# Kernel tuning notes

Measured on AMD Instinct MI355X. Metric: run time of the kernel, lower is better.

The kernel has to match this reference:

```python
import jax, jax.numpy as jnp
import numpy as np

N_NODES = 100000
N_EDGES = 50000
NNZ = 1600000
C_IN = 128
C_OUT = 128
BN_EPS = 1e-5


def setup_inputs() -> dict:
    key = jax.random.key(0)
    k_x, k_ni, k_ei, k_w, k_W, k_b = jax.random.split(key, 6)
    x = jax.random.normal(k_x, (N_NODES, C_IN), dtype=jnp.float32)
    node_idx = jax.random.randint(k_ni, (NNZ,), 0, N_NODES, dtype=jnp.int64)
    edge_idx = jax.random.randint(k_ei, (NNZ,), 0, N_EDGES, dtype=jnp.int64)
    hyperedge_index = jnp.stack([node_idx, edge_idx], axis=0)  # [2, nnz]
    hyperedge_weight = jax.random.uniform(k_w, (N_EDGES,), dtype=jnp.float32)
    W = jax.random.normal(k_W, (C_IN, C_OUT), dtype=jnp.float32) * (1.0 / np.sqrt(C_IN))
    b = jax.random.normal(k_b, (C_OUT,), dtype=jnp.float32) * 0.02
    gamma = jnp.ones((C_OUT,), dtype=jnp.float32)
    beta = jnp.zeros((C_OUT,), dtype=jnp.float32)
    return {"x": x, "hyperedge_index": hyperedge_index,
            "hyperedge_weight": hyperedge_weight, "W": W, "b": b,
            "gamma": gamma, "beta": beta}


def reference(x, hyperedge_index, hyperedge_weight, W, b, gamma, beta):
    # HypergraphConv (PyG semantics): out = D^{-1} H B^{-1} H^T (X W) + b
    # D_v = sum_{e: v in e} w_e  (hyperedge weights enter via node degree),
    # B_e = |e| (number of incident nodes).
    N = x.shape[0]
    E = hyperedge_weight.shape[0]
    node_idx = hyperedge_index[0]
    edge_idx = hyperedge_index[1]

    xt = x @ W  # [N, C_out]

    # Node degree D (weighted) and hyperedge degree B.
    D = jax.ops.segment_sum(hyperedge_weight[edge_idx], node_idx, num_segments=N)
    D_inv = jnp.where(D > 0, 1.0 / D, 0.0)  # inf -> 0
    Bdeg = jax.ops.segment_sum(jnp.ones(edge_idx.shape, dtype=xt.dtype),
                               edge_idx, num_segments=E)
    B_inv = jnp.where(Bdeg > 0, 1.0 / Bdeg, 0.0)

    # node -> hyperedge aggregation: e = B^{-1} sum_{v in e} xt_v
    e_feat = jax.ops.segment_sum(xt[node_idx], edge_idx, num_segments=E)
    e_feat = e_feat * B_inv[:, None]  # [E, C_out]

    # hyperedge -> node aggregation: out_v = D^{-1} sum_{e ni v} e_feat_e
    out = jax.ops.segment_sum(e_feat[edge_idx], node_idx, num_segments=N)
    out = out * D_inv[:, None] + b  # [N, C_out]

    # BatchNorm (training-mode batch statistics over nodes)
    mean = jnp.mean(out, axis=0)
    var = jnp.mean(jnp.square(out - mean), axis=0)  # biased, as BatchNorm1d
    out = (out - mean) * jax.lax.rsqrt(var + BN_EPS) * gamma + beta

    # SiLU activation
    out = out * jax.nn.sigmoid(out)
    # NOTE: original code computes `x = out + x` for the skip but returns `out`,
    # so the skip is a no-op; we faithfully return `out` (use_skip=False here).
    return out
```

## Files before the change

### kernel.cpp

```cpp
#include <hip/hip_runtime.h>
#include <cstdint>
#include <cstddef>

#define CC 128
#define LOG_FINE 7
#define FINE 128
#define CAPE 6144
#define CAPV 3072
#define BIN_TILE 8192

typedef __attribute__((ext_vector_type(8))) short bf16x8;
typedef __attribute__((ext_vector_type(4))) float f32x4;

__device__ __forceinline__ unsigned f2b(float f) {
    const unsigned u = __float_as_uint(f);
    return (u + 0x7fffu + ((u >> 16) & 1u)) >> 16;
}
__device__ __forceinline__ float b2f_lo(unsigned u) { return __uint_as_float(u << 16); }
__device__ __forceinline__ float b2f_hi(unsigned u) { return __uint_as_float(u & 0xffff0000u); }

__global__ __launch_bounds__(512) void prep(const int* __restrict__ nidx,
                                            const int* __restrict__ eidx,
                                            int* __restrict__ curE,
                                            int* __restrict__ curV,
                                            unsigned* __restrict__ binnedE,
                                            unsigned* __restrict__ binnedV,
                                            int nnz, int nbE, int nbV, int nbin,
                                            const float4* __restrict__ xin,
                                            uint2* __restrict__ xh, int n4) {
    __shared__ int cntE[512], gposE[512];
    __shared__ int cntV[1024], gposV[1024];
    const int tid = threadIdx.x;
    if (blockIdx.x >= (unsigned)nbin) {
        const int bid = blockIdx.x - nbin;
        const int nblk = gridDim.x - nbin;
        for (int i = bid * 512 + tid; i < n4; i += nblk * 512) {
            const float4 v = xin[i];
            xh[i] = make_uint2(f2b(v.x) | (f2b(v.y) << 16), f2b(v.z) | (f2b(v.w) << 16));
        }
        return;
    }
    for (int i = tid; i < nbE; i += 512) cntE[i] = 0;
    for (int i = tid; i < nbV; i += 512) cntV[i] = 0;
    __syncthreads();
    const int base = blockIdx.x * BIN_TILE;
    int pE[16], rE[16], pV[16], rV[16];
#pragma unroll
    for (int j = 0; j < 16; ++j) {
        const int i = base + tid + j * 512;
        if (i < nnz) {
            const int e = eidx[i], v = nidx[i];
            const int bE = e >> LOG_FINE, bV = v >> LOG_FINE;
            rE[j] = (bE << 16) | atomicAdd(&cntE[bE], 1);
            pE[j] = (v << LOG_FINE) | (e & (FINE - 1));
            rV[j] = (bV << 16) | atomicAdd(&cntV[bV], 1);
            pV[j] = (e << LOG_FINE) | (v & (FINE - 1));
        } else { rE[j] = -1; rV[j] = -1; }
    }
    __syncthreads();
    for (int i = tid; i < nbE; i += 512) {
        const int c = cntE[i];
        gposE[i] = (c > 0) ? atomicAdd(&curE[i], c) : 0;
    }
    for (int i = tid; i < nbV; i += 512) {
        const int c = cntV[i];
        gposV[i] = (c > 0) ? atomicAdd(&curV[i], c) : 0;
    }
    __syncthreads();
#pragma unroll
    for (int j = 0; j < 16; ++j) {
        if (rE[j] >= 0) {
            const int b = rE[j] >> 16;
            binnedE[(size_t)b * CAPE + gposE[b] + (rE[j] & 0xffff)] = (unsigned)pE[j];
        }
        if (rV[j] >= 0) {
            const int b = rV[j] >> 16;
            binnedV[(size_t)b * CAPV + gposV[b] + (rV[j] & 0xffff)] = (unsigned)pV[j];
        }
    }
}

__global__ __launch_bounds__(256) void bfrag_prep(const float* __restrict__ W,
                                                  uint4* __restrict__ Bfrag) {
    const int idx = blockIdx.x * 256 + threadIdx.x;
    if (idx >= 2048) return;
    const int lane = idx & 63, t = idx >> 6;
    const int kk = t >> 3, nt = t & 7;
    const int k0 = kk * 32 + (lane >> 4) * 8;
    const int n = nt * 16 + (lane & 15);
    unsigned r[4];
#pragma unroll
    for (int p = 0; p < 4; ++p) {
        const float w0 = W[(size_t)(k0 + 2 * p) * CC + n];
        const float w1 = W[(size_t)(k0 + 2 * p + 1) * CC + n];
        r[p] = f2b(w0) | (f2b(w1) << 16);
    }
    Bfrag[idx] = make_uint4(r[0], r[1], r[2], r[3]);
}

__global__ __launch_bounds__(512) void fill_fineE(const int* __restrict__ cur,
                                                  unsigned* __restrict__ binned,
                                                  int2* __restrict__ rows, int nrows) {
    __shared__ unsigned vals[CAPE];
    __shared__ int scnt[FINE], soff[FINE], sscan[FINE];
    const int tid = threadIdx.x;
    const int b = blockIdx.x;
    const int base = b * CAPE;
    const int cnt = cur[b];
    for (int i = tid; i < cnt; i += 512) vals[i] = binned[base + i];
    if (tid < FINE) scnt[tid] = 0;
    __syncthreads();
    for (int i = tid; i < cnt; i += 512) atomicAdd(&scnt[vals[i] & (FINE - 1)], 1);
    __syncthreads();
    if (tid < FINE) sscan[tid] = scnt[tid];
    __syncthreads();
#pragma unroll
    for (int d = 1; d < FINE; d <<= 1) {
        int t = 0;
        if (tid >= d && tid < FINE) t = sscan[tid - d];
        __syncthreads();
        if (tid < FINE) sscan[tid] += t;
        __syncthreads();
    }
    if (tid < FINE) {
        const int excl = sscan[tid] - scnt[tid];
        soff[tid] = excl;
        const int row = (b << LOG_FINE) + tid;
        if (row < nrows) rows[row] = make_int2(base + excl, base + excl + scnt[tid]);
    }
    __syncthreads();
    for (int i = tid; i < cnt; i += 512) {
        const unsigned p = vals[i];
        const int slot = (int)(p & (FINE - 1));
        const int pos = base + atomicAdd(&soff[slot], 1);
        binned[pos] = p >> LOG_FINE;
    }
}

__global__ __launch_bounds__(512) void fillV_gather(const int* __restrict__ curV,
                                                    unsigned* __restrict__ binnedV,
                                                    const float* __restrict__ hw,
                                                    int2* __restrict__ rowsV,
                                                    float* __restrict__ Dinv,
                                                    int N, int nbV,
                                                    const int2* __restrict__ rowsE,
                                                    const unsigned* __restrict__ binnedE,
                                                    const uint4* __restrict__ xh4,
                                                    uint4* __restrict__ eraw4, int E) {
    __shared__ unsigned vals[CAPV];
    __shared__ int scnt[FINE], soff[FINE], sscan[FINE];
    __shared__ float sd[FINE];
    const int tid = threadIdx.x;
    if (blockIdx.x < (unsigned)nbV) {
        const int b = blockIdx.x;
        const int base = b * CAPV;
        const int cnt = curV[b];
        for (int i = tid; i < cnt; i += 512) vals[i] = binnedV[base + i];
        if (tid < FINE) { scnt[tid] = 0; sd[tid] = 0.f; }
        __syncthreads();
        for (int i = tid; i < cnt; i += 512) atomicAdd(&scnt[vals[i] & (FINE - 1)], 1);
        __syncthreads();
        if (tid < FINE) sscan[tid] = scnt[tid];
        __syncthreads();
#pragma unroll
        for (int d = 1; d < FINE; d <<= 1) {
            int t = 0;
            if (tid >= d && tid < FINE) t = sscan[tid - d];
            __syncthreads();
            if (tid < FINE) sscan[tid] += t;
            __syncthreads();
        }
        if (tid < FINE) {
            const int excl = sscan[tid] - scnt[tid];
            soff[tid] = excl;
            const int row = (b << LOG_FINE) + tid;
            if (row < N) rowsV[row] = make_int2(base + excl, base + excl + scnt[tid]);
        }
        __syncthreads();
        for (int i = tid; i < cnt; i += 512) {
            const unsigned p = vals[i];
            const int slot = (int)(p & (FINE - 1));
            const int e = (int)(p >> LOG_FINE);
            const int pos = base + atomicAdd(&soff[slot], 1);
            binnedV[pos] = (unsigned)e;
            atomicAdd(&sd[slot], hw[e]);
        }
        __syncthreads();
        if (tid < FINE) {
            const int row = (b << LOG_FINE) + tid;
            if (row < N) {
                const float d = sd[tid];
                Dinv[row] = (d > 0.f) ? 1.f / d : 0.f;
            }
        }
        return;
    }
    const int sub = tid >> 5;
    const int half = (tid >> 4) & 1;
    const int q = tid & 15;
    const int e = (blockIdx.x - nbV) * 16 + sub;
    if (e >= E) return;
    const int2 st = rowsE[e];
    const int s = st.x, t = st.y;
    float a[8];
#pragma unroll
    for (int k = 0; k < 8; ++k) a[k] = 0.f;
    int j = s;
    for (; j + 7 < t; j += 8) {
        const int v0 = (int)binnedE[j + 0 + half];
        const int v1 = (int)binnedE[j + 2 + half];
        const int v2 = (int)binnedE[j + 4 + half];
        const int v3 = (int)binnedE[j + 6 + half];
        const uint4 u0 = xh4[(size_t)v0 * 16 + q];
        const uint4 u1 = xh4[(size_t)v1 * 16 + q];
        const uint4 u2 = xh4[(size_t)v2 * 16 + q];
        const uint4 u3 = xh4[(size_t)v3 * 16 + q];
        a[0] += b2f_lo(u0.x) + b2f_lo(u1.x) + b2f_lo(u2.x) + b2f_lo(u3.x);
        a[1] += b2f_hi(u0.x) + b2f_hi(u1.x) + b2f_hi(u2.x) + b2f_hi(u3.x);
        a[2] += b2f_lo(u0.y) + b2f_lo(u1.y) + b2f_lo(u2.y) + b2f_lo(u3.y);
        a[3] += b2f_hi(u0.y) + b2f_hi(u1.y) + b2f_hi(u2.y) + b2f_hi(u3.y);
        a[4] += b2f_lo(u0.z) + b2f_lo(u1.z) + b2f_lo(u2.z) + b2f_lo(u3.z);
        a[5] += b2f_hi(u0.z) + b2f_hi(u1.z) + b2f_hi(u2.z) + b2f_hi(u3.z);
        a[6] += b2f_lo(u0.w) + b2f_lo(u1.w) + b2f_lo(u2.w) + b2f_lo(u3.w);
        a[7] += b2f_hi(u0.w) + b2f_hi(u1.w) + b2f_hi(u2.w) + b2f_hi(u3.w);
    }
    for (; j + 1 < t; j += 2) {
        const int v0 = (int)binnedE[j + half];
        const uint4 u = xh4[(size_t)v0 * 16 + q];
        a[0] += b2f_lo(u.x); a[1] += b2f_hi(u.x);
        a[2] += b2f_lo(u.y); a[3] += b2f_hi(u.y);
        a[4] += b2f_lo(u.z); a[5] += b2f_hi(u.z);
        a[6] += b2f_lo(u.w); a[7] += b2f_hi(u.w);
    }
    if (j < t && half == 0) {
        const uint4 u = xh4[(size_t)binnedE[j] * 16 + q];
        a[0] += b2f_lo(u.x); a[1] += b2f_hi(u.x);
        a[2] += b2f_lo(u.y); a[3] += b2f_hi(u.y);
        a[4] += b2f_lo(u.z); a[5] += b2f_hi(u.z);
        a[6] += b2f_lo(u.w); a[7] += b2f_hi(u.w);
    }
#pragma unroll
    for (int k = 0; k < 8; ++k) a[k] += __shfl_xor(a[k], 16);
    if (half == 0) {
        const float binv = (t > s) ? 1.f / (float)(t - s) : 0.f;
#pragma unroll
        for (int k = 0; k < 8; ++k) a[k] *= binv;
        uint4 o;
        o.x = f2b(a[0]) | (f2b(a[1]) << 16);
        o.y = f2b(a[2]) | (f2b(a[3]) << 16);
        o.z = f2b(a[4]) | (f2b(a[5]) << 16);
        o.w = f2b(a[6]) | (f2b(a[7]) << 16);
        eraw4[(size_t)e * 16 + q] = o;
    }
}

__global__ __launch_bounds__(256) void mm_mfma(const uint4* __restrict__ A4,
                                               const uint4* __restrict__ Bfrag,
                                               unsigned short* __restrict__ Out, int M) {
    const int lane = threadIdx.x & 63;
    const int wave = threadIdx.x >> 6;
    const int row0 = blockIdx.x * 64 + wave * 16;
    const int g = lane >> 4;
    const int c = lane & 15;
    const int arow = row0 + c;
    uint4 a[4];
#pragma unroll
    for (int kk = 0; kk < 4; ++kk) {
        a[kk] = (arow < M) ? A4[(size_t)arow * 16 + kk * 4 + g]
                           : make_uint4(0u, 0u, 0u, 0u);
    }
    f32x4 acc[8];
#pragma unroll
    for (int nt = 0; nt < 8; ++nt) acc[nt] = (f32x4){0.f, 0.f, 0.f, 0.f};
#pragma unroll
    for (int nt = 0; nt < 8; ++nt) {
#pragma unroll
        for (int kk = 0; kk < 4; ++kk) {
            const uint4 bv = Bfrag[(kk * 8 + nt) * 64 + lane];
            acc[nt] = __builtin_amdgcn_mfma_f32_16x16x32_bf16(
                *(const bf16x8*)&a[kk], *(const bf16x8*)&bv, acc[nt], 0, 0, 0);
        }
    }
#pragma unroll
    for (int nt = 0; nt < 8; ++nt) {
#pragma unroll
        for (int r = 0; r < 4; ++r) {
            const int row = row0 + g * 4 + r;
            if (row < M) Out[(size_t)row * CC + nt * 16 + c] = (unsigned short)f2b(acc[nt][r]);
        }
    }
}

__global__ __launch_bounds__(256) void gather_e2n_bn(const int2* __restrict__ rows,
                                                     const unsigned* __restrict__ lst,
                                                     const uint4* __restrict__ ef4,
                                                     const float* __restrict__ Dinv,
                                                     const float* __restrict__ b,
                                                     uint4* __restrict__ oh,
                                                     float* __restrict__ copies, int N) {
    __shared__ float bl[8][256];
    const int tid = threadIdx.x;
    for (int i = tid; i < 2048; i += 256) ((float*)bl)[i] = 0.f;
    __syncthreads();
    const int sub = tid >> 5;
    const int half = (tid >> 4) & 1;
    const int q = tid & 15;
    const int v = blockIdx.x * 8 + sub;
    if (v < N) {
        const int2 st = rows[v];
        const int s = st.x, t = st.y;
        float a[8];
#pragma unroll
        for (int k = 0; k < 8; ++k) a[k] = 0.f;
        int j = s;
        for (; j + 7 < t; j += 8) {
            const int e0 = (int)lst[j + 0 + half];
            const int e1 = (int)lst[j + 2 + half];
            const int e2 = (int)lst[j + 4 + half];
            const int e3 = (int)lst[j + 6 + half];
            const uint4 u0 = ef4[(size_t)e0 * 16 + q];
            const uint4 u1 = ef4[(size_t)e1 * 16 + q];
            const uint4 u2 = ef4[(size_t)e2 * 16 + q];
            const uint4 u3 = ef4[(size_t)e3 * 16 + q];
            a[0] += b2f_lo(u0.x) + b2f_lo(u1.x) + b2f_lo(u2.x) + b2f_lo(u3.x);
            a[1] += b2f_hi(u0.x) + b2f_hi(u1.x) + b2f_hi(u2.x) + b2f_hi(u3.x);
            a[2] += b2f_lo(u0.y) + b2f_lo(u1.y) + b2f_lo(u2.y) + b2f_lo(u3.y);
            a[3] += b2f_hi(u0.y) + b2f_hi(u1.y) + b2f_hi(u2.y) + b2f_hi(u3.y);
            a[4] += b2f_lo(u0.z) + b2f_lo(u1.z) + b2f_lo(u2.z) + b2f_lo(u3.z);
            a[5] += b2f_hi(u0.z) + b2f_hi(u1.z) + b2f_hi(u2.z) + b2f_hi(u3.z);
            a[6] += b2f_lo(u0.w) + b2f_lo(u1.w) + b2f_lo(u2.w) + b2f_lo(u3.w);
            a[7] += b2f_hi(u0.w) + b2f_hi(u1.w) + b2f_hi(u2.w) + b2f_hi(u3.w);
        }
        for (; j + 1 < t; j += 2) {
            const int e0 = (int)lst[j + half];
            const uint4 u = ef4[(size_t)e0 * 16 + q];
            a[0] += b2f_lo(u.x); a[1] += b2f_hi(u.x);
            a[2] += b2f_lo(u.y); a[3] += b2f_hi(u.y);
            a[4] += b2f_lo(u.z); a[5] += b2f_hi(u.z);
            a[6] += b2f_lo(u.w); a[7] += b2f_hi(u.w);
        }
        if (j < t && half == 0) {
            const uint4 u = ef4[(size_t)lst[j] * 16 + q];
            a[0] += b2f_lo(u.x); a[1] += b2f_hi(u.x);
            a[2] += b2f_lo(u.y); a[3] += b2f_hi(u.y);
            a[4] += b2f_lo(u.z); a[5] += b2f_hi(u.z);
            a[6] += b2f_lo(u.w); a[7] += b2f_hi(u.w);
        }
#pragma unroll
        for (int k = 0; k < 8; ++k) a[k] += __shfl_xor(a[k], 16);
        if (half == 0) {
            const float dinv = Dinv[v];
            const float4 b0 = *(const float4*)&b[8 * q];
            const float4 b1 = *(const float4*)&b[8 * q + 4];
            float o[8];
            o[0] = a[0] * dinv + b0.x; o[1] = a[1] * dinv + b0.y;
            o[2] = a[2] * dinv + b0.z; o[3] = a[3] * dinv + b0.w;
            o[4] = a[4] * dinv + b1.x; o[5] = a[5] * dinv + b1.y;
            o[6] = a[6] * dinv + b1.z; o[7] = a[7] * dinv + b1.w;
            uint4 ov;
            ov.x = f2b(o[0]) | (f2b(o[1]) << 16);
            ov.y = f2b(o[2]) | (f2b(o[3]) << 16);
            ov.z = f2b(o[4]) | (f2b(o[5]) << 16);
            ov.w = f2b(o[6]) | (f2b(o[7]) << 16);
            oh[(size_t)v * 16 + q] = ov;
            *(float4*)&bl[sub][8 * q]       = make_float4(o[0], o[1], o[2], o[3]);
            *(float4*)&bl[sub][8 * q + 4]   = make_float4(o[4], o[5], o[6], o[7]);
            *(float4*)&bl[sub][128 + 8 * q] = make_float4(o[0] * o[0], o[1] * o[1],
                                                          o[2] * o[2], o[3] * o[3]);
            *(float4*)&bl[sub][132 + 8 * q] = make_float4(o[4] * o[4], o[5] * o[5],
                                                          o[6] * o[6], o[7] * o[7]);
        }
    }
    __syncthreads();
    float s = 0.f;
#pragma unroll
    for (int i = 0; i < 8; ++i) s += bl[i][tid];
    atomicAdd(&copies[(blockIdx.x & 63) * 256 + tid], s);
}

__global__ __launch_bounds__(256) void bn_silu(const uint2* __restrict__ oh2,
                                               const float* __restrict__ copies,
                                               const float* __restrict__ gamma,
                                               const float* __restrict__ beta,
                                               float* __restrict__ out, int N) {
    __shared__ float sl[256];
    const int tid = threadIdx.x;
    float s = 0.f;
#pragma unroll 8
    for (int i = 0; i < 64; ++i) s += copies[i * 256 + tid];
    sl[tid] = s;
    __syncthreads();
    const int sub = tid >> 5;
    const int lane = tid & 31;
    const int c4 = lane * 4;
    const float invN = 1.0f / (float)N;
    float g[4], bb[4];
#pragma unroll
    for (int k = 0; k < 4; ++k) {
        const float mean = sl[c4 + k] * invN;
        float var = sl[128 + c4 + k] * invN - mean * mean;
        var = fmaxf(var, 0.f);
        const float istd = rsqrtf(var + 1e-5f);
        g[k] = gamma[c4 + k] * istd;
        bb[k] = beta[c4 + k] - mean * g[k];
    }
    for (int v = blockIdx.x * 8 + sub; v < N; v += gridDim.x * 8) {
        const uint2 u = oh2[(size_t)v * 32 + lane];
        float y[4];
        y[0] = b2f_lo(u.x); y[1] = b2f_hi(u.x);
        y[2] = b2f_lo(u.y); y[3] = b2f_hi(u.y);
        float4 o;
#pragma unroll
        for (int k = 0; k < 4; ++k) {
            const float z = y[k] * g[k] + bb[k];
            (&o.x)[k] = z / (1.f + __expf(-z));
        }
        *(float4*)&out[(size_t)v * CC + c4] = o;
    }
}

extern "C" void kernel_launch(void* const* d_in, const int* in_sizes, int n_in,
                              void* d_out, int out_size, void* d_ws, size_t ws_size,
                              hipStream_t stream) {
    const float* x     = (const float*)d_in[0];
    const int*   hidx  = (const int*)d_in[1];
    const float* hw    = (const float*)d_in[2];
    const float* W     = (const float*)d_in[3];
    const float* b     = (const float*)d_in[4];
    const float* gamma = (const float*)d_in[5];
    const float* beta  = (const float*)d_in[6];

    const int N   = in_sizes[0] / CC;
    const int nnz = in_sizes[1] / 2;
    const int E   = in_sizes[2];

    const int* nidx = hidx;
    const int* eidx = hidx + nnz;

    float* out = (float*)d_out;

    const int nbE = (E + FINE - 1) / FINE;
    const int nbV = (N + FINE - 1) / FINE;

    unsigned* ws      = (unsigned*)d_ws;
    unsigned* xh      = ws;
    unsigned* eraw    = xh + (size_t)N * 64;
    unsigned* efeat   = eraw + (size_t)E * 64;
    int2*     rowsE   = (int2*)(efeat + (size_t)E * 64);
    int2*     rowsV   = rowsE + E;
    float*    Dinv    = (float*)(rowsV + N);
    float*    copies  = Dinv + N;
    int*      curE    = (int*)(copies + 64 * 256);
    int*      curV    = curE + nbE;
    unsigned* binnedE = (unsigned*)(curV + nbV);
    unsigned* binnedV = binnedE + (size_t)nbE * CAPE;
    uintptr_t bfaddr  = (uintptr_t)(binnedV + (size_t)nbV * CAPV);
    uint4*    Bfrag   = (uint4*)((bfaddr + 15) & ~(uintptr_t)15);

    hipMemsetAsync(copies, 0, (64 * 256 + (size_t)nbE + nbV) * sizeof(int), stream);

    const int nbin = (nnz + BIN_TILE - 1) / BIN_TILE;
    const int ncvt = 256;
    prep<<<nbin + ncvt, 512, 0, stream>>>(nidx, eidx, curE, curV, binnedE, binnedV,
                                          nnz, nbE, nbV, nbin,
                                          (const float4*)x, (uint2*)xh, N * CC / 4);
    bfrag_prep<<<8, 256, 0, stream>>>(W, Bfrag);

    fill_fineE<<<nbE, 512, 0, stream>>>(curE, binnedE, rowsE, E);

    fillV_gather<<<nbV + (E + 15) / 16, 512, 0, stream>>>(
        curV, binnedV, hw, rowsV, Dinv, N, nbV,
        rowsE, binnedE, (const uint4*)xh, (uint4*)eraw, E);

    mm_mfma<<<(E + 63) / 64, 256, 0, stream>>>((const uint4*)eraw, Bfrag,
                                               (unsigned short*)efeat, E);

    gather_e2n_bn<<<(N + 7) / 8, 256, 0, stream>>>(rowsV, binnedV, (const uint4*)efeat,
                                                   Dinv, b, (uint4*)xh, copies, N);

    bn_silu<<<1024, 256, 0, stream>>>((const uint2*)xh, copies, gamma, beta, out, N);
}
```

Before: 215.8 us.

## Fuse node-to-edge gather with MFMA matmul and merge fine-binning kernels

Result: slower. 220.6 us (+2.2%).

```diff
diff --git a/kernel.cpp b/kernel.cpp
--- a/kernel.cpp
+++ b/kernel.cpp
@@ -7,7 +7,7 @@
 #define FINE 128
 #define CAPE 6144
 #define CAPV 3072
-#define BIN_TILE 8192
+#define BIN_TILE 4096
 
 typedef __attribute__((ext_vector_type(8))) short bf16x8;
 typedef __attribute__((ext_vector_type(4))) float f32x4;
@@ -44,9 +44,9 @@
     for (int i = tid; i < nbV; i += 512) cntV[i] = 0;
     __syncthreads();
     const int base = blockIdx.x * BIN_TILE;
-    int pE[16], rE[16], pV[16], rV[16];
-#pragma unroll
-    for (int j = 0; j < 16; ++j) {
+    int pE[8], rE[8], pV[8], rV[8];
+#pragma unroll
+    for (int j = 0; j < 8; ++j) {
         const int i = base + tid + j * 512;
         if (i < nnz) {
             const int e = eidx[i], v = nidx[i];
@@ -68,7 +68,7 @@
     }
     __syncthreads();
 #pragma unroll
-    for (int j = 0; j < 16; ++j) {
+    for (int j = 0; j < 8; ++j) {
         if (rE[j] >= 0) {
             const int b = rE[j] >> 16;
             binnedE[(size_t)b * CAPE + gposE[b] + (rE[j] & 0xffff)] = (unsigned)pE[j];
@@ -98,17 +98,29 @@
     Bfrag[idx] = make_uint4(r[0], r[1], r[2], r[3]);
 }
 
-__global__ __launch_bounds__(512) void fill_fineE(const int* __restrict__ cur,
-                                                  unsigned* __restrict__ binned,
-                                                  int2* __restrict__ rows, int nrows) {
+__global__ __launch_bounds__(512) void fill_all(const int* __restrict__ curE,
+                                                const int* __restrict__ curV,
+                                                unsigned* __restrict__ binnedE,
+                                                unsigned* __restrict__ binnedV,
+                                                const float* __restrict__ hw,
+                                                int2* __restrict__ rowsE,
+                                                int2* __restrict__ rowsV,
+                                                float* __restrict__ Dinv,
+                                                int E, int N, int nbE) {
     __shared__ unsigned vals[CAPE];
     __shared__ int scnt[FINE], soff[FINE], sscan[FINE];
+    __shared__ float sd[FINE];
     const int tid = threadIdx.x;
-    const int b = blockIdx.x;
-    const int base = b * CAPE;
-    const int cnt = cur[b];
+    const bool isE = (blockIdx.x < (unsigned)nbE);
+    const int b = isE ? blockIdx.x : blockIdx.x - nbE;
+    const int cap = isE ? CAPE : CAPV;
+    const int base = b * cap;
+    const int cnt = isE ? curE[b] : curV[b];
+    unsigned* binned = isE ? binnedE : binnedV;
+    int2* rows = isE ? rowsE : rowsV;
+    const int nrows = isE ? E : N;
     for (int i = tid; i < cnt; i += 512) vals[i] = binned[base + i];
-    if (tid < FINE) scnt[tid] = 0;
+    if (tid < FINE) { scnt[tid] = 0; sd[tid] = 0.f; }
     __syncthreads();
     for (int i = tid; i < cnt; i += 512) atomicAdd(&scnt[vals[i] & (FINE - 1)], 1);
     __syncthreads();
@@ -129,60 +141,20 @@
         if (row < nrows) rows[row] = make_int2(base + excl, base + excl + scnt[tid]);
     }
     __syncthreads();
-    for (int i = tid; i < cnt; i += 512) {
-        const unsigned p = vals[i];
-        const int slot = (int)(p & (FINE - 1));
-        const int pos = base + atomicAdd(&soff[slot], 1);
-        binned[pos] = p >> LOG_FINE;
-    }
-}
-
-__global__ __launch_bounds__(512) void fillV_gather(const int* __restrict__ curV,
-                                                    unsigned* __restrict__ binnedV,
-                                                    const float* __restrict__ hw,
-                                                    int2* __restrict__ rowsV,
-                                                    float* __restrict__ Dinv,
-                                                    int N, int nbV,
-                                                    const int2* __restrict__ rowsE,
-                                                    const unsigned* __restrict__ binnedE,
-                                                    const uint4* __restrict__ xh4,
-                                                    uint4* __restrict__ eraw4, int E) {
-    __shared__ unsigned vals[CAPV];
-    __shared__ int scnt[FINE], soff[FINE], sscan[FINE];
-    __shared__ float sd[FINE];
-    const int tid = threadIdx.x;
-    if (blockIdx.x < (unsigned)nbV) {
-        const int b = blockIdx.x;
-        const int base = b * CAPV;
-        const int cnt = curV[b];
-        for (int i = tid; i < cnt; i += 512) vals[i] = binnedV[base + i];
-        if (tid < FINE) { scnt[tid] = 0; sd[tid] = 0.f; }
-        __syncthreads();
-        for (int i = tid; i < cnt; i += 512) atomicAdd(&scnt[vals[i] & (FINE - 1)], 1);
-        __syncthreads();
-        if (tid < FINE) sscan[tid] = scnt[tid];
-        __syncthreads();
-#pragma unroll
-        for (int d = 1; d < FINE; d <<= 1) {
-            int t = 0;
-            if (tid >= d && tid < FINE) t = sscan[tid - d];
-            __syncthreads();
-            if (tid < FINE) sscan[tid] += t;
-            __syncthreads();
-        }
-        if (tid < FINE) {
-            const int excl = sscan[tid] - scnt[tid];
-            soff[tid] = excl;
-            const int row = (b << LOG_FINE) + tid;
-            if (row < N) rowsV[row] = make_int2(base + excl, base + excl + scnt[tid]);
-        }
-        __syncthreads();
+    if (isE) {
+        for (int i = tid; i < cnt; i += 512) {
+            const unsigned p = vals[i];
+            const int slot = (int)(p & (FINE - 1));
+            const int pos = base + atomicAdd(&soff[slot], 1);
+            binned[pos] = p >> LOG_FINE;
+        }
+    } else {
         for (int i = tid; i < cnt; i += 512) {
             const unsigned p = vals[i];
             const int slot = (int)(p & (FINE - 1));
             const int e = (int)(p >> LOG_FINE);
             const int pos = base + atomicAdd(&soff[slot], 1);
-            binnedV[pos] = (unsigned)e;
+            binned[pos] = (unsigned)e;
             atomicAdd(&sd[slot], hw[e]);
         }
         __syncthreads();
@@ -193,51 +165,61 @@
                 Dinv[row] = (d > 0.f) ? 1.f / d : 0.f;
             }
         }
-        return;
-    }
+    }
+}
+
+__global__ __launch_bounds__(512) void n2e_mm(const int2* __restrict__ rowsE,
+                                              const unsigned* __restrict__ binnedE,
+                                              const uint4* __restrict__ xh4,
+                                              const uint4* __restrict__ Bfrag,
+                                              unsigned short* __restrict__ efeat, int E) {
+    __shared__ uint4 tile[16][17];
+    const int tid = threadIdx.x;
     const int sub = tid >> 5;
     const int half = (tid >> 4) & 1;
     const int q = tid & 15;
-    const int e = (blockIdx.x - nbV) * 16 + sub;
-    if (e >= E) return;
-    const int2 st = rowsE[e];
-    const int s = st.x, t = st.y;
+    const int e = blockIdx.x * 16 + sub;
     float a[8];
 #pragma unroll
     for (int k = 0; k < 8; ++k) a[k] = 0.f;
-    int j = s;
-    for (; j + 7 < t; j += 8) {
-        const int v0 = (int)binnedE[j + 0 + half];
-        const int v1 = (int)binnedE[j + 2 + half];
-        const int v2 = (int)binnedE[j + 4 + half];
-        const int v3 = (int)binnedE[j + 6 + half];
-        const uint4 u0 = xh4[(size_t)v0 * 16 + q];
-        const uint4 u1 = xh4[(size_t)v1 * 16 + q];
-        const uint4 u2 = xh4[(size_t)v2 * 16 + q];
-        const uint4 u3 = xh4[(size_t)v3 * 16 + q];
-        a[0] += b2f_lo(u0.x) + b2f_lo(u1.x) + b2f_lo(u2.x) + b2f_lo(u3.x);
-        a[1] += b2f_hi(u0.x) + b2f_hi(u1.x) + b2f_hi(u2.x) + b2f_hi(u3.x);
-        a[2] += b2f_lo(u0.y) + b2f_lo(u1.y) + b2f_lo(u2.y) + b2f_lo(u3.y);
-        a[3] += b2f_hi(u0.y) + b2f_hi(u1.y) + b2f_hi(u2.y) + b2f_hi(u3.y);
-        a[4] += b2f_lo(u0.z) + b2f_lo(u1.z) + b2f_lo(u2.z) + b2f_lo(u3.z);
-        a[5] += b2f_hi(u0.z) + b2f_hi(u1.z) + b2f_hi(u2.z) + b2f_hi(u3.z);
-        a[6] += b2f_lo(u0.w) + b2f_lo(u1.w) + b2f_lo(u2.w) + b2f_lo(u3.w);
-        a[7] += b2f_hi(u0.w) + b2f_hi(u1.w) + b2f_hi(u2.w) + b2f_hi(u3.w);
-    }
-    for (; j + 1 < t; j += 2) {
-        const int v0 = (int)binnedE[j + half];
-        const uint4 u = xh4[(size_t)v0 * 16 + q];
-        a[0] += b2f_lo(u.x); a[1] += b2f_hi(u.x);
-        a[2] += b2f_lo(u.y); a[3] += b2f_hi(u.y);
-        a[4] += b2f_lo(u.z); a[5] += b2f_hi(u.z);
-        a[6] += b2f_lo(u.w); a[7] += b2f_hi(u.w);
-    }
-    if (j < t && half == 0) {
-        const uint4 u = xh4[(size_t)binnedE[j] * 16 + q];
-        a[0] += b2f_lo(u.x); a[1] += b2f_hi(u.x);
-        a[2] += b2f_lo(u.y); a[3] += b2f_hi(u.y);
-        a[4] += b2f_lo(u.z); a[5] += b2f_hi(u.z);
-        a[6] += b2f_lo(u.w); a[7] += b2f_hi(u.w);
+    int s = 0, t = 0;
+    if (e < E) {
+        const int2 st = rowsE[e];
+        s = st.x; t = st.y;
+        int j = s;
+        for (; j + 7 < t; j += 8) {
+            const int v0 = (int)binnedE[j + 0 + half];
+            const int v1 = (int)binnedE[j + 2 + half];
+            const int v2 = (int)binnedE[j + 4 + half];
+            const int v3 = (int)binnedE[j + 6 + half];
+            const uint4 u0 = xh4[(size_t)v0 * 16 + q];
+            const uint4 u1 = xh4[(size_t)v1 * 16 + q];
+            const uint4 u2 = xh4[(size_t)v2 * 16 + q];
+            const uint4 u3 = xh4[(size_t)v3 * 16 + q];
+            a[0] += b2f_lo(u0.x) + b2f_lo(u1.x) + b2f_lo(u2.x) + b2f_lo(u3.x);
+            a[1] += b2f_hi(u0.x) + b2f_hi(u1.x) + b2f_hi(u2.x) + b2f_hi(u3.x);
+            a[2] += b2f_lo(u0.y) + b2f_lo(u1.y) + b2f_lo(u2.y) + b2f_lo(u3.y);
+            a[3] += b2f_hi(u0.y) + b2f_hi(u1.y) + b2f_hi(u2.y) + b2f_hi(u3.y);
+            a[4] += b2f_lo(u0.z) + b2f_lo(u1.z) + b2f_lo(u2.z) + b2f_lo(u3.z);
+            a[5] += b2f_hi(u0.z) + b2f_hi(u1.z) + b2f_hi(u2.z) + b2f_hi(u3.z);
+            a[6] += b2f_lo(u0.w) + b2f_lo(u1.w) + b2f_lo(u2.w) + b2f_lo(u3.w);
+            a[7] += b2f_hi(u0.w) + b2f_hi(u1.w) + b2f_hi(u2.w) + b2f_hi(u3.w);
+        }
+        for (; j + 1 < t; j += 2) {
+            const int v0 = (int)binnedE[j + half];
+            const uint4 u = xh4[(size_t)v0 * 16 + q];
+            a[0] += b2f_lo(u.x); a[1] += b2f_hi(u.x);
+            a[2] += b2f_lo(u.y); a[3] += b2f_hi(u.y);
+            a[4] += b2f_lo(u.z); a[5] += b2f_hi(u.z);
+            a[6] += b2f_lo(u.w); a[7] += b2f_hi(u.w);
+        }
+        if (j < t && half == 0) {
+            const uint4 u = xh4[(size_t)binnedE[j] * 16 + q];
+            a[0] += b2f_lo(u.x); a[1] += b2f_hi(u.x);
+            a[2] += b2f_lo(u.y); a[3] += b2f_hi(u.y);
+            a[4] += b2f_lo(u.z); a[5] += b2f_hi(u.z);
+            a[6] += b2f_lo(u.w); a[7] += b2f_hi(u.w);
+        }
     }
 #pragma unroll
     for (int k = 0; k < 8; ++k) a[k] += __shfl_xor(a[k], 16);
@@ -250,44 +232,27 @@
         o.y = f2b(a[2]) | (f2b(a[3]) << 16);
         o.z = f2b(a[4]) | (f2b(a[5]) << 16);
         o.w = f2b(a[6]) | (f2b(a[7]) << 16);
-        eraw4[(size_t)e * 16 + q] = o;
-    }
-}
-
-__global__ __launch_bounds__(256) void mm_mfma(const uint4* __restrict__ A4,
-                                               const uint4* __restrict__ Bfrag,
-                                               unsigned short* __restrict__ Out, int M) {
-    const int lane = threadIdx.x & 63;
-    const int wave = threadIdx.x >> 6;
-    const int row0 = blockIdx.x * 64 + wave * 16;
+        tile[sub][q] = o;
+    }
+    __syncthreads();
+    const int w = tid >> 6;
+    const int lane = tid & 63;
     const int g = lane >> 4;
     const int c = lane & 15;
-    const int arow = row0 + c;
-    uint4 a[4];
+    uint4 af[4];
+#pragma unroll
+    for (int kk = 0; kk < 4; ++kk) af[kk] = tile[lane & 15][kk * 4 + g];
+    f32x4 acc = (f32x4){0.f, 0.f, 0.f, 0.f};
 #pragma unroll
     for (int kk = 0; kk < 4; ++kk) {
-        a[kk] = (arow < M) ? A4[(size_t)arow * 16 + kk * 4 + g]
-                           : make_uint4(0u, 0u, 0u, 0u);
-    }
-    f32x4 acc[8];
-#pragma unroll
-    for (int nt = 0; nt < 8; ++nt) acc[nt] = (f32x4){0.f, 0.f, 0.f, 0.f};
-#pragma unroll
-    for (int nt = 0; nt < 8; ++nt) {
-#pragma unroll
-        for (int kk = 0; kk < 4; ++kk) {
-            const uint4 bv = Bfrag[(kk * 8 + nt) * 64 + lane];
-            acc[nt] = __builtin_amdgcn_mfma_f32_16x16x32_bf16(
-                *(const bf16x8*)&a[kk], *(const bf16x8*)&bv, acc[nt], 0, 0, 0);
-        }
-    }
-#pragma unroll
-    for (int nt = 0; nt < 8; ++nt) {
-#pragma unroll
-        for (int r = 0; r < 4; ++r) {
-            const int row = row0 + g * 4 + r;
-            if (row < M) Out[(size_t)row * CC + nt * 16 + c] = (unsigned short)f2b(acc[nt][r]);
-        }
+        const uint4 bv = Bfrag[(kk * 8 + w) * 64 + lane];
+        acc = __builtin_amdgcn_mfma_f32_16x16x32_bf16(
+            *(const bf16x8*)&af[kk], *(const bf16x8*)&bv, acc, 0, 0, 0);
+    }
+#pragma unroll
+    for (int r = 0; r < 4; ++r) {
+        const int row = blockIdx.x * 16 + g * 4 + r;
+        if (row < E) efeat[(size_t)row * CC + w * 16 + c] = (unsigned short)f2b(acc[r]);
     }
 }
 
@@ -444,8 +409,7 @@
 
     unsigned* ws      = (unsigned*)d_ws;
     unsigned* xh      = ws;
-    unsigned* eraw    = xh + (size_t)N * 64;
-    unsigned* efeat   = eraw + (size_t)E * 64;
+    unsigned* efeat   = xh + (size_t)N * 64;
     int2*     rowsE   = (int2*)(efeat + (size_t)E * 64);
     int2*     rowsV   = rowsE + E;
     float*    Dinv    = (float*)(rowsV + N);
@@ -466,14 +430,11 @@
                                           (const float4*)x, (uint2*)xh, N * CC / 4);
     bfrag_prep<<<8, 256, 0, stream>>>(W, Bfrag);
 
-    fill_fineE<<<nbE, 512, 0, stream>>>(curE, binnedE, rowsE, E);
-
-    fillV_gather<<<nbV + (E + 15) / 16, 512, 0, stream>>>(
-        curV, binnedV, hw, rowsV, Dinv, N, nbV,
-        rowsE, binnedE, (const uint4*)xh, (uint4*)eraw, E);
-
-    mm_mfma<<<(E + 63) / 64, 256, 0, stream>>>((const uint4*)eraw, Bfrag,
-                                               (unsigned short*)efeat, E);
+    fill_all<<<nbE + nbV, 512, 0, stream>>>(curE, curV, binnedE, binnedV, hw,
+                                            rowsE, rowsV, Dinv, E, N, nbE);
+
+    n2e_mm<<<(E + 15) / 16, 512, 0, stream>>>(rowsE, binnedE, (const uint4*)xh,
+                                              Bfrag, (unsigned short*)efeat, E);
 
     gather_e2n_bn<<<(N + 7) / 8, 256, 0, stream>>>(rowsV, binnedV, (const uint4*)efeat,
                                                    Dinv, b, (uint4*)xh, copies, N);
```
